# Performance work log

Measured on AMD Instinct MI355X. Metric: run time of the kernel, lower is better.

The kernel has to match this reference:

```python
import jax, jax.numpy as jnp
import numpy as np

N_NODES = 40000
N_EDGES = 640000
IN_DIM, H_DIM, OUT_DIM = 128, 128, 64


def setup_inputs() -> dict:
    key = jax.random.key(0)
    ks = jax.random.split(key, 16)
    x = jax.random.normal(ks[0], (N_NODES, IN_DIM), dtype=jnp.float32)
    edge_index = jax.random.randint(ks[1], (2, N_EDGES), 0, N_NODES, dtype=jnp.int64)
    dims = [(IN_DIM, H_DIM), (H_DIM, H_DIM), (H_DIM, OUT_DIM)]
    inp = {"x": x, "edge_index": edge_index}
    for l, (di, do) in enumerate(dims):
        s = 1.0 / np.sqrt(di)
        inp[f"Wr{l}"] = jax.random.uniform(ks[2 + 3 * l], (di, do), jnp.float32, -s, s)  # lin_rel weight
        inp[f"br{l}"] = jax.random.uniform(ks[3 + 3 * l], (do,), jnp.float32, -s, s)     # lin_rel bias
        inp[f"Ws{l}"] = jax.random.uniform(ks[4 + 3 * l], (di, do), jnp.float32, -s, s)  # lin_root weight (no bias)
    return inp


def _graph_conv(x, src, dst, Wr, br, Ws):
    # PyG GraphConv (aggr='add'): out = lin_rel(sum_{j in N(i)} x_j) + lin_root(x_i)
    agg = jax.ops.segment_sum(x[src], dst, num_segments=N_NODES)  # [N, d_in]
    return agg @ Wr + br + x @ Ws


def reference(x, edge_index, Wr0, br0, Ws0, Wr1, br1, Ws1, Wr2, br2, Ws2):
    src, dst = edge_index[0], edge_index[1]
    h = x
    for Wr, br, Ws in ((Wr0, br0, Ws0), (Wr1, br1, Ws1), (Wr2, br2, Ws2)):
        h = _graph_conv(h, src, dst, Wr, br, Ws)
        h = jax.nn.relu(h)
        # dropout p=0 / eval mode -> identity
    return jax.nn.log_softmax(h, axis=1)
```

## Files before the change

kernel.cpp:

```cpp
#include <hip/hip_runtime.h>
#include <hip/hip_bf16.h>


#define N_NODES 40000
#define N_EDGES 640000
#define PAD_NODES 40064
#define DEG_CAP   40960
#define ROW_CAP   64

typedef float v4f __attribute__((ext_vector_type(4)));
typedef float v2f __attribute__((ext_vector_type(2)));
typedef short short8 __attribute__((ext_vector_type(8)));

__device__ inline unsigned short f2b(float f) {
    unsigned u = __float_as_uint(f);
    return (unsigned short)((u + 0x7fffu + ((u >> 16) & 1u)) >> 16);
}

__global__ __launch_bounds__(256) void prep_kernel(const float* __restrict__ Wr0, const float* __restrict__ Ws0,
                                                   const float* __restrict__ Wr1, const float* __restrict__ Ws1,
                                                   const float* __restrict__ Wr2, const float* __restrict__ Ws2,
                                                   unsigned short* __restrict__ Wt0,
                                                   unsigned short* __restrict__ Wt1,
                                                   unsigned short* __restrict__ Wt2,
                                                   int* __restrict__ deg) {
    int tid = blockIdx.x * 256 + threadIdx.x;
    if (tid < DEG_CAP / 4) {
        ((int4*)deg)[tid] = make_int4(0, 0, 0, 0);
    } else {
        int t = tid - DEG_CAP / 4;
        if (t < 32768) {
            int n = t >> 7, k = t & 127;
            const float* W = (n < 128) ? Wr0 : Ws0;
            Wt0[t] = f2b(W[k * 128 + (n & 127)]);
        } else if (t < 65536) {
            int u = t - 32768;
            int n = u >> 7, k = u & 127;
            const float* W = (n < 128) ? Wr1 : Ws1;
            Wt1[u] = f2b(W[k * 128 + (n & 127)]);
        } else if (t < 81920) {
            int u = t - 65536;
            int n = u >> 7, k = u & 127;
            const float* W = (n < 64) ? Wr2 : Ws2;
            Wt2[u] = f2b(W[k * 64 + (n & 63)]);
        }
    }
}

__global__ __launch_bounds__(256) void place_kernel(const int* __restrict__ src,
                                                    const int* __restrict__ dst,
                                                    int* __restrict__ deg,
                                                    int* __restrict__ esrc) {
    int e = blockIdx.x * 256 + threadIdx.x;
    if (e < N_EDGES) {
        int d = dst[e];
        int r = atomicAdd(&deg[d], 1);
        if (r < ROW_CAP) esrc[(size_t)d * ROW_CAP + r] = src[e];
    }
}

template <int DO, bool F32>
__global__ __launch_bounds__(256, 3) void mm_kernel(const void* __restrict__ Ain,
                                                    const unsigned short* __restrict__ Wt,
                                                    unsigned short* __restrict__ T,
                                                    unsigned short* __restrict__ S) {
    __shared__ unsigned short As[128 * 64];
    __shared__ unsigned short Bs[128 * 64];

    const int tid = threadIdx.x;
    const int m0  = blockIdx.x * 128;
    const int n0  = blockIdx.y * 128;

    const int wave = tid >> 6;
    const int lane = tid & 63;
    const int wr   = (wave >> 1) * 64;
    const int wc   = (wave & 1) * 64;
    const int qm   = lane & 15;
    const int k8   = (lane >> 4) * 8;

    v4f acc[4][4];
#pragma unroll
    for (int i = 0; i < 4; i++)
#pragma unroll
        for (int j = 0; j < 4; j++) acc[i][j] = (v4f)(0.0f);

#pragma unroll
    for (int half = 0; half < 2; half++) {
        if (F32) {
            const float4* Xg = (const float4*)Ain;
#pragma unroll
            for (int i = 0; i < 8; i++) {
                int idx = i * 256 + tid;
                int row = idx >> 4, c4 = idx & 15;
                int gr = m0 + row;
                if (gr > N_NODES - 1) gr = N_NODES - 1;
                float4 v = Xg[(size_t)gr * 32 + half * 16 + c4];
                uint2 p;
                p.x = (unsigned)f2b(v.x) | ((unsigned)f2b(v.y) << 16);
                p.y = (unsigned)f2b(v.z) | ((unsigned)f2b(v.w) << 16);
                ((uint2*)As)[idx] = p;
            }
        } else {
            const unsigned short* Ab = (const unsigned short*)Ain;
#pragma unroll
            for (int i = 0; i < 4; i++) {
                int idx = i * 256 + tid;
                int row = idx >> 3, c8 = idx & 7;
                ((uint4*)As)[idx] =
                    *(const uint4*)(Ab + (size_t)(m0 + row) * 128 + half * 64 + c8 * 8);
            }
        }
        {
#pragma unroll
            for (int i = 0; i < 4; i++) {
                int idx = i * 256 + tid;
                int row = idx >> 3, c8 = idx & 7;
                ((uint4*)Bs)[idx] =
                    *(const uint4*)(Wt + (size_t)(n0 + row) * 128 + half * 64 + c8 * 8);
            }
        }
        __syncthreads();

#pragma unroll
        for (int ks = 0; ks < 2; ks++) {
            short8 af[4], bf[4];
#pragma unroll
            for (int i = 0; i < 4; i++) {
                af[i] = *(const short8*)(const void*)(As + (wr + i * 16 + qm) * 64 + ks * 32 + k8);
                bf[i] = *(const short8*)(const void*)(Bs + (wc + i * 16 + qm) * 64 + ks * 32 + k8);
            }
#pragma unroll
            for (int mi = 0; mi < 4; mi++)
#pragma unroll
                for (int ni = 0; ni < 4; ni++)
                    acc[mi][ni] = __builtin_amdgcn_mfma_f32_16x16x32_bf16(af[mi], bf[ni], acc[mi][ni], 0, 0, 0);
        }
        __syncthreads();
    }

#pragma unroll
    for (int mi = 0; mi < 4; mi++) {
        const int nodeBase = m0 + wr + mi * 16 + ((lane >> 4) << 2);
#pragma unroll
        for (int r = 0; r < 4; r++) {
            const int node = nodeBase + r;
            if (node <= N_NODES) {
                const bool real = (node < N_NODES);
#pragma unroll
                for (int ni = 0; ni < 4; ni++) {
                    const int c = wc + ni * 16 + qm;
                    const unsigned short hv = real ? f2b(acc[mi][ni][r]) : (unsigned short)0;
                    if (DO == 128) {
                        (blockIdx.y ? S : T)[(size_t)node * 128 + c] = hv;
                    } else {
                        if (c < 64) T[(size_t)node * 64 + c] = hv;
                        else        S[(size_t)node * 64 + (c - 64)] = hv;
                    }
                }
            }
        }
    }
}

__device__ inline void addp(v2f* a, uint4 q) {
    v2f t0 = { __uint_as_float(q.x << 16), __uint_as_float(q.x & 0xffff0000u) };
    v2f t1 = { __uint_as_float(q.y << 16), __uint_as_float(q.y & 0xffff0000u) };
    v2f t2 = { __uint_as_float(q.z << 16), __uint_as_float(q.z & 0xffff0000u) };
    v2f t3 = { __uint_as_float(q.w << 16), __uint_as_float(q.w & 0xffff0000u) };
    a[0] += t0; a[1] += t1; a[2] += t2; a[3] += t3;
}

template <int DO, bool LAST>
__global__ __launch_bounds__(256) void aggregate_kernel(const unsigned short* __restrict__ T,
                                                        const unsigned short* __restrict__ S,
                                                        const float* __restrict__ br,
                                                        const int* __restrict__ deg,
                                                        const int* __restrict__ esrc,
                                                        unsigned short* __restrict__ Hout,
                                                        float* __restrict__ Fout) {
    constexpr int TPN = DO / 8;
    constexpr int G   = 256 / TPN;
    const int lane = threadIdx.x % TPN;
    const int n    = blockIdx.x * G + threadIdx.x / TPN;

    int cnt = deg[n];
    if (cnt > ROW_CAP) cnt = ROW_CAP;
    const int* erow = esrc + (size_t)n * ROW_CAP;
    const uint4* T4 = (const uint4*)T;

    const uint4  sv = ((const uint4*)S)[(size_t)n * TPN + lane];
    const float4 b0 = ((const float4*)br)[lane * 2];
    const float4 b1 = ((const float4*)br)[lane * 2 + 1];

    v2f acc[4];
    acc[0] = (v2f)(0.0f); acc[1] = (v2f)(0.0f);
    acc[2] = (v2f)(0.0f); acc[3] = (v2f)(0.0f);

    for (int o = 0; o < cnt; o += 8) {
        int4 i0 = *(const int4*)(erow + o);
        int4 i1 = *(const int4*)(erow + o + 4);
        i0.x = (o + 0 < cnt) ? i0.x : N_NODES;
        i0.y = (o + 1 < cnt) ? i0.y : N_NODES;
        i0.z = (o + 2 < cnt) ? i0.z : N_NODES;
        i0.w = (o + 3 < cnt) ? i0.w : N_NODES;
        i1.x = (o + 4 < cnt) ? i1.x : N_NODES;
        i1.y = (o + 5 < cnt) ? i1.y : N_NODES;
        i1.z = (o + 6 < cnt) ? i1.z : N_NODES;
        i1.w = (o + 7 < cnt) ? i1.w : N_NODES;
        uint4 q0 = T4[(size_t)i0.x * TPN + lane];
        uint4 q1 = T4[(size_t)i0.y * TPN + lane];
        uint4 q2 = T4[(size_t)i0.z * TPN + lane];
        uint4 q3 = T4[(size_t)i0.w * TPN + lane];
        uint4 q4 = T4[(size_t)i1.x * TPN + lane];
        uint4 q5 = T4[(size_t)i1.y * TPN + lane];
        uint4 q6 = T4[(size_t)i1.z * TPN + lane];
        uint4 q7 = T4[(size_t)i1.w * TPN + lane];
        addp(acc, q0); addp(acc, q1); addp(acc, q2); addp(acc, q3);
        addp(acc, q4); addp(acc, q5); addp(acc, q6); addp(acc, q7);
    }
    addp(acc, sv);

    float v[8];
    v[0] = fmaxf(acc[0].x + b0.x, 0.f); v[1] = fmaxf(acc[0].y + b0.y, 0.f);
    v[2] = fmaxf(acc[1].x + b0.z, 0.f); v[3] = fmaxf(acc[1].y + b0.w, 0.f);
    v[4] = fmaxf(acc[2].x + b1.x, 0.f); v[5] = fmaxf(acc[2].y + b1.y, 0.f);
    v[6] = fmaxf(acc[3].x + b1.z, 0.f); v[7] = fmaxf(acc[3].y + b1.w, 0.f);

    if (LAST) {
        float m = v[0];
#pragma unroll
        for (int i = 1; i < 8; i++) m = fmaxf(m, v[i]);
#pragma unroll
        for (int off = 4; off; off >>= 1) m = fmaxf(m, __shfl_xor(m, off, 64));
        float es = 0.f;
#pragma unroll
        for (int i = 0; i < 8; i++) es += expf(v[i] - m);
#pragma unroll
        for (int off = 4; off; off >>= 1) es += __shfl_xor(es, off, 64);
        float lse = m + logf(es);
        float4 o0 = make_float4(v[0] - lse, v[1] - lse, v[2] - lse, v[3] - lse);
        float4 o1 = make_float4(v[4] - lse, v[5] - lse, v[6] - lse, v[7] - lse);
        ((float4*)Fout)[(size_t)n * 16 + lane * 2]     = o0;
        ((float4*)Fout)[(size_t)n * 16 + lane * 2 + 1] = o1;
    } else {
        uint4 o;
        o.x = (unsigned)f2b(v[0]) | ((unsigned)f2b(v[1]) << 16);
        o.y = (unsigned)f2b(v[2]) | ((unsigned)f2b(v[3]) << 16);
        o.z = (unsigned)f2b(v[4]) | ((unsigned)f2b(v[5]) << 16);
        o.w = (unsigned)f2b(v[6]) | ((unsigned)f2b(v[7]) << 16);
        ((uint4*)Hout)[(size_t)n * TPN + lane] = o;
    }
}


extern "C" void kernel_launch(void* const* d_in, const int* in_sizes, int n_in,
                              void* d_out, int out_size, void* d_ws, size_t ws_size,
                              hipStream_t stream) {
    const float* x    = (const float*)d_in[0];
    const int*   eidx = (const int*)d_in[1];
    const float* Wr0  = (const float*)d_in[2];
    const float* br0  = (const float*)d_in[3];
    const float* Ws0  = (const float*)d_in[4];
    const float* Wr1  = (const float*)d_in[5];
    const float* br1  = (const float*)d_in[6];
    const float* Ws1  = (const float*)d_in[7];
    const float* Wr2  = (const float*)d_in[8];
    const float* br2  = (const float*)d_in[9];
    const float* Ws2  = (const float*)d_in[10];
    float* out = (float*)d_out;

    const int* src = eidx;
    const int* dst = eidx + N_EDGES;

    auto align = [](size_t v) { return (v + 255) & ~(size_t)255; };
    char* w = (char*)d_ws;
    int* deg  = (int*)w;  w += align(sizeof(int) * DEG_CAP);
    int* esrc = (int*)w;  w += align(sizeof(int) * (size_t)N_NODES * ROW_CAP);
    unsigned short* H1b = (unsigned short*)w;  w += align(2ull * PAD_NODES * 128);
    unsigned short* H2b = (unsigned short*)w;  w += align(2ull * PAD_NODES * 128);
    unsigned short* Wt0 = (unsigned short*)w;  w += align(2ull * 256 * 128);
    unsigned short* Wt1 = (unsigned short*)w;  w += align(2ull * 256 * 128);
    unsigned short* Wt2 = (unsigned short*)w;  w += align(2ull * 128 * 128);
    unsigned short* T   = (unsigned short*)w;  w += align(2ull * PAD_NODES * 128);
    unsigned short* Sb  = (unsigned short*)w;  w += align(2ull * PAD_NODES * 128);
    (void)ws_size; (void)n_in; (void)in_sizes; (void)out_size;

    prep_kernel<<<(DEG_CAP / 4 + 81920 + 255) / 256, 256, 0, stream>>>(
        Wr0, Ws0, Wr1, Ws1, Wr2, Ws2, Wt0, Wt1, Wt2, deg);

    place_kernel<<<(N_EDGES + 255) / 256, 256, 0, stream>>>(src, dst, deg, esrc);

    mm_kernel<128, true><<<dim3(PAD_NODES / 128, 2), 256, 0, stream>>>(x, Wt0, T, Sb);
    aggregate_kernel<128, false><<<N_NODES / 16, 256, 0, stream>>>(T, Sb, br0, deg, esrc, H1b, nullptr);

    mm_kernel<128, false><<<dim3(PAD_NODES / 128, 2), 256, 0, stream>>>(H1b, Wt1, T, Sb);
    aggregate_kernel<128, false><<<N_NODES / 16, 256, 0, stream>>>(T, Sb, br1, deg, esrc, H2b, nullptr);

    mm_kernel<64, false><<<dim3(PAD_NODES / 128, 1), 256, 0, stream>>>(H2b, Wt2, T, Sb);
    aggregate_kernel<64, true><<<N_NODES / 32, 256, 0, stream>>>(T, Sb, br2, deg, esrc, nullptr, out);
}
```

Measured before the change: 212.0 us.

## Fuse edge placement into first GEMM launch and store edge sources as u16

```diff
diff --git a/kernel.cpp b/kernel.cpp
--- a/kernel.cpp
+++ b/kernel.cpp
@@ -7,6 +7,8 @@
 #define PAD_NODES 40064
 #define DEG_CAP   40960
 #define ROW_CAP   64
+#define MM1_BLOCKS 626
+#define PLACE_BLOCKS 2500
 
 typedef float v4f __attribute__((ext_vector_type(4)));
 typedef float v2f __attribute__((ext_vector_type(2)));
@@ -47,29 +49,15 @@
     }
 }
 
-__global__ __launch_bounds__(256) void place_kernel(const int* __restrict__ src,
-                                                    const int* __restrict__ dst,
-                                                    int* __restrict__ deg,
-                                                    int* __restrict__ esrc) {
-    int e = blockIdx.x * 256 + threadIdx.x;
-    if (e < N_EDGES) {
-        int d = dst[e];
-        int r = atomicAdd(&deg[d], 1);
-        if (r < ROW_CAP) esrc[(size_t)d * ROW_CAP + r] = src[e];
-    }
-}
-
 template <int DO, bool F32>
-__global__ __launch_bounds__(256, 3) void mm_kernel(const void* __restrict__ Ain,
-                                                    const unsigned short* __restrict__ Wt,
-                                                    unsigned short* __restrict__ T,
-                                                    unsigned short* __restrict__ S) {
-    __shared__ unsigned short As[128 * 64];
-    __shared__ unsigned short Bs[128 * 64];
-
+__device__ __forceinline__ void mm_body(const void* __restrict__ Ain,
+                                        const unsigned short* __restrict__ Wt,
+                                        unsigned short* __restrict__ T,
+                                        unsigned short* __restrict__ S,
+                                        unsigned short* __restrict__ As,
+                                        unsigned short* __restrict__ Bs,
+                                        int m0, int n0) {
     const int tid = threadIdx.x;
-    const int m0  = blockIdx.x * 128;
-    const int n0  = blockIdx.y * 128;
 
     const int wave = tid >> 6;
     const int lane = tid & 63;
@@ -151,13 +139,47 @@
                     const int c = wc + ni * 16 + qm;
                     const unsigned short hv = real ? f2b(acc[mi][ni][r]) : (unsigned short)0;
                     if (DO == 128) {
-                        (blockIdx.y ? S : T)[(size_t)node * 128 + c] = hv;
+                        (n0 ? S : T)[(size_t)node * 128 + c] = hv;
                     } else {
                         if (c < 64) T[(size_t)node * 64 + c] = hv;
                         else        S[(size_t)node * 64 + (c - 64)] = hv;
                     }
                 }
             }
+        }
+    }
+}
+
+template <int DO, bool F32>
+__global__ __launch_bounds__(256, 3) void mm_kernel(const void* __restrict__ Ain,
+                                                    const unsigned short* __restrict__ Wt,
+                                                    unsigned short* __restrict__ T,
+                                                    unsigned short* __restrict__ S) {
+    __shared__ unsigned short As[128 * 64];
+    __shared__ unsigned short Bs[128 * 64];
+    mm_body<DO, F32>(Ain, Wt, T, S, As, Bs, blockIdx.x * 128, blockIdx.y * 128);
+}
+
+__global__ __launch_bounds__(256, 3) void mm1_place_kernel(const float* __restrict__ x,
+                                                           const unsigned short* __restrict__ Wt0,
+                                                           unsigned short* __restrict__ T,
+                                                           unsigned short* __restrict__ S,
+                                                           const int* __restrict__ src,
+                                                           const int* __restrict__ dst,
+                                                           int* __restrict__ deg,
+                                                           unsigned short* __restrict__ esrc) {
+    if (blockIdx.x < MM1_BLOCKS) {
+        __shared__ unsigned short As[128 * 64];
+        __shared__ unsigned short Bs[128 * 64];
+        const int m0 = ((int)blockIdx.x >> 1) * 128;
+        const int n0 = ((int)blockIdx.x & 1) * 128;
+        mm_body<128, true>(x, Wt0, T, S, As, Bs, m0, n0);
+    } else {
+        int e = ((int)blockIdx.x - MM1_BLOCKS) * 256 + threadIdx.x;
+        if (e < N_EDGES) {
+            int d = dst[e];
+            int r = atomicAdd(&deg[d], 1);
+            if (r < ROW_CAP) esrc[(size_t)d * ROW_CAP + r] = (unsigned short)src[e];
         }
     }
 }
@@ -175,7 +197,7 @@
                                                         const unsigned short* __restrict__ S,
                                                         const float* __restrict__ br,
                                                         const int* __restrict__ deg,
-                                                        const int* __restrict__ esrc,
+                                                        const unsigned short* __restrict__ esrc,
                                                         unsigned short* __restrict__ Hout,
                                                         float* __restrict__ Fout) {
     constexpr int TPN = DO / 8;
@@ -185,7 +207,7 @@
 
     int cnt = deg[n];
     if (cnt > ROW_CAP) cnt = ROW_CAP;
-    const int* erow = esrc + (size_t)n * ROW_CAP;
+    const unsigned short* erow = esrc + (size_t)n * ROW_CAP;
     const uint4* T4 = (const uint4*)T;
 
     const uint4  sv = ((const uint4*)S)[(size_t)n * TPN + lane];
@@ -197,24 +219,27 @@
     acc[2] = (v2f)(0.0f); acc[3] = (v2f)(0.0f);
 
     for (int o = 0; o < cnt; o += 8) {
-        int4 i0 = *(const int4*)(erow + o);
-        int4 i1 = *(const int4*)(erow + o + 4);
-        i0.x = (o + 0 < cnt) ? i0.x : N_NODES;
-        i0.y = (o + 1 < cnt) ? i0.y : N_NODES;
-        i0.z = (o + 2 < cnt) ? i0.z : N_NODES;
-        i0.w = (o + 3 < cnt) ? i0.w : N_NODES;
-        i1.x = (o + 4 < cnt) ? i1.x : N_NODES;
-        i1.y = (o + 5 < cnt) ? i1.y : N_NODES;
-        i1.z = (o + 6 < cnt) ? i1.z : N_NODES;
-        i1.w = (o + 7 < cnt) ? i1.w : N_NODES;
-        uint4 q0 = T4[(size_t)i0.x * TPN + lane];
-        uint4 q1 = T4[(size_t)i0.y * TPN + lane];
-        uint4 q2 = T4[(size_t)i0.z * TPN + lane];
-        uint4 q3 = T4[(size_t)i0.w * TPN + lane];
-        uint4 q4 = T4[(size_t)i1.x * TPN + lane];
-        uint4 q5 = T4[(size_t)i1.y * TPN + lane];
-        uint4 q6 = T4[(size_t)i1.z * TPN + lane];
-        uint4 q7 = T4[(size_t)i1.w * TPN + lane];
+        uint4 iv = *(const uint4*)(erow + o);
+        unsigned j0 = iv.x & 0xffffu, j1 = iv.x >> 16;
+        unsigned j2 = iv.y & 0xffffu, j3 = iv.y >> 16;
+        unsigned j4 = iv.z & 0xffffu, j5 = iv.z >> 16;
+        unsigned j6 = iv.w & 0xffffu, j7 = iv.w >> 16;
+        j0 = (o + 0 < cnt) ? j0 : N_NODES;
+        j1 = (o + 1 < cnt) ? j1 : N_NODES;
+        j2 = (o + 2 < cnt) ? j2 : N_NODES;
+        j3 = (o + 3 < cnt) ? j3 : N_NODES;
+        j4 = (o + 4 < cnt) ? j4 : N_NODES;
+        j5 = (o + 5 < cnt) ? j5 : N_NODES;
+        j6 = (o + 6 < cnt) ? j6 : N_NODES;
+        j7 = (o + 7 < cnt) ? j7 : N_NODES;
+        uint4 q0 = T4[(size_t)j0 * TPN + lane];
+        uint4 q1 = T4[(size_t)j1 * TPN + lane];
+        uint4 q2 = T4[(size_t)j2 * TPN + lane];
+        uint4 q3 = T4[(size_t)j3 * TPN + lane];
+        uint4 q4 = T4[(size_t)j4 * TPN + lane];
+        uint4 q5 = T4[(size_t)j5 * TPN + lane];
+        uint4 q6 = T4[(size_t)j6 * TPN + lane];
+        uint4 q7 = T4[(size_t)j7 * TPN + lane];
         addp(acc, q0); addp(acc, q1); addp(acc, q2); addp(acc, q3);
         addp(acc, q4); addp(acc, q5); addp(acc, q6); addp(acc, q7);
     }
@@ -274,8 +299,9 @@
 
     auto align = [](size_t v) { return (v + 255) & ~(size_t)255; };
     char* w = (char*)d_ws;
-    int* deg  = (int*)w;  w += align(sizeof(int) * DEG_CAP);
-    int* esrc = (int*)w;  w += align(sizeof(int) * (size_t)N_NODES * ROW_CAP);
+    int* deg  = (int*)w;             w += align(sizeof(int) * DEG_CAP);
+    unsigned short* esrc = (unsigned short*)w;
+    w += align(sizeof(unsigned short) * (size_t)N_NODES * ROW_CAP);
     unsigned short* H1b = (unsigned short*)w;  w += align(2ull * PAD_NODES * 128);
     unsigned short* H2b = (unsigned short*)w;  w += align(2ull * PAD_NODES * 128);
     unsigned short* Wt0 = (unsigned short*)w;  w += align(2ull * 256 * 128);
@@ -288,9 +314,8 @@
     prep_kernel<<<(DEG_CAP / 4 + 81920 + 255) / 256, 256, 0, stream>>>(
         Wr0, Ws0, Wr1, Ws1, Wr2, Ws2, Wt0, Wt1, Wt2, deg);
 
-    place_kernel<<<(N_EDGES + 255) / 256, 256, 0, stream>>>(src, dst, deg, esrc);
-
-    mm_kernel<128, true><<<dim3(PAD_NODES / 128, 2), 256, 0, stream>>>(x, Wt0, T, Sb);
+    mm1_place_kernel<<<MM1_BLOCKS + PLACE_BLOCKS, 256, 0, stream>>>(
+        x, Wt0, T, Sb, src, dst, deg, esrc);
     aggregate_kernel<128, false><<<N_NODES / 16, 256, 0, stream>>>(T, Sb, br0, deg, esrc, H1b, nullptr);
 
     mm_kernel<128, false><<<dim3(PAD_NODES / 128, 2), 256, 0, stream>>>(H1b, Wt1, T, Sb);
```

Result: slower. 217.8 us (+2.7%).
